# Optimization experiments

Measured on AMD Instinct MI355X. Metric: run time of the kernel, lower is better.

The kernel has to match this reference:

```python
import jax, jax.numpy as jnp
import numpy as np

TOKENS_PER_LAYER = 16  # v in rearrange 'b l (a v) -> b l a v'


def setup_inputs() -> dict:
    key = jax.random.key(0)
    k1, k2 = jax.random.split(key)
    vocab, embed_dim = 1024, 256
    x = jax.random.normal(k1, (64, 32, embed_dim * TOKENS_PER_LAYER), dtype=jnp.float32)
    # nn.Embedding init: uniform(-1/vocab, 1/vocab)
    emb_weight = jax.random.uniform(k2, (vocab, embed_dim), dtype=jnp.float32,
                                    minval=-1.0 / vocab, maxval=1.0 / vocab)
    return {"x": x, "emb_weight": emb_weight}


def reference(x, emb_weight):
    v = TOKENS_PER_LAYER
    b, l, av = x.shape
    a = av // v  # embed_dim
    # rearrange 'b l (a v) -> b l a v'
    z = x.reshape(b, l, a, v)
    # rearrange 'b l a v -> (b l v) a'
    z_flat = z.transpose(0, 1, 3, 2).reshape(b * l * v, a)
    # pairwise squared L2 distance via sum-of-squares + GEMM: [N, vocab]
    dist = (jnp.sum(z_flat * z_flat, axis=1, keepdims=True)
            + jnp.sum(emb_weight * emb_weight, axis=1)
            - 2.0 * (z_flat @ emb_weight.T))
    tokens = jnp.argmin(dist, axis=-1)  # [N] int
    # embedding gather, then rearrange '(b l v) e -> b l e v'
    z_q = emb_weight[tokens].reshape(b, l, v, a).transpose(0, 1, 3, 2)
    # straight-through decoder input: z + sg(z_q - z)
    decoder_input = z + jax.lax.stop_gradient(z_q - z)
    tokens = tokens.reshape(b, l, v)
    return z_q, decoder_input, tokens
```

## Files before the change

kernel.cpp:

```cpp
#include <hip/hip_runtime.h>


#define A_DIM 256
#define VOCAB 1024
#define NROWS 32768
#define ZQ_ELEMS ((size_t)8388608)
#define TAU_C 3.0e-4f
#define TAU_F 2.0e-4f

typedef _Float16 f16x8 __attribute__((ext_vector_type(8)));
typedef float f32x4 __attribute__((ext_vector_type(4)));

#define WS_EHT   ((size_t)0)
#define WS_ZH    ((size_t)524288)
#define WS_ESQ   ((size_t)17301504)
#define WS_ZSQ   ((size_t)17305600)
#define WS_NEED  ((size_t)17436672)


__global__ __launch_bounds__(256) void prep_fused(const float* __restrict__ x,
                                                  const float* __restrict__ emb,
                                                  _Float16* __restrict__ zh,
                                                  float* __restrict__ zsq,
                                                  float* __restrict__ esq,
                                                  _Float16* __restrict__ eht) {
    __shared__ float raw[A_DIM * 17];
    const int tid = threadIdx.x;
    if (blockIdx.x >= 2048) {
        const int blk = blockIdx.x - 2048;
        const int j = blk * 16 + (tid & 15);
        const int sub = tid >> 4;
        const float4* row = (const float4*)(emb + (size_t)j * A_DIM);
        #pragma unroll
        for (int t = 0; t < 2; ++t) {
            int kb = sub * 2 + t;
            float4 e0 = row[kb * 2], e1 = row[kb * 2 + 1];
            f16x8 hh;
            hh[0] = (_Float16)e0.x; hh[1] = (_Float16)e0.y; hh[2] = (_Float16)e0.z; hh[3] = (_Float16)e0.w;
            hh[4] = (_Float16)e1.x; hh[5] = (_Float16)e1.y; hh[6] = (_Float16)e1.z; hh[7] = (_Float16)e1.w;
            *(f16x8*)(eht + ((size_t)kb * 1024 + j) * 8) = hh;
        }
        if (sub == 0) {
            double s = 0.0;
            #pragma unroll 4
            for (int t = 0; t < A_DIM / 4; ++t) {
                float4 f = row[t];
                float sx = f.x * f.x, sy = f.y * f.y, sz = f.z * f.z, sw = f.w * f.w;
                s += (double)sx + (double)sy + (double)sz + (double)sw;
            }
            esq[j] = (float)s;
        }
        return;
    }
    const int bl = blockIdx.x;
    #pragma unroll
    for (int t = 0; t < 4; ++t) {
        int f4 = tid * 4 + t * 1024;
        float4 val = *(const float4*)(x + (size_t)bl * 4096 + f4);
        int a = f4 >> 4, v0 = f4 & 15;
        raw[a * 17 + v0 + 0] = val.x;
        raw[a * 17 + v0 + 1] = val.y;
        raw[a * 17 + v0 + 2] = val.z;
        raw[a * 17 + v0 + 3] = val.w;
    }
    __syncthreads();
    #pragma unroll
    for (int t = 0; t < 16; ++t) {
        int f = tid + t * 256;
        int v = f >> 8, a = f & 255;
        zh[((size_t)bl * 16 + v) * 256 + a] = (_Float16)raw[a * 17 + v];
    }
    if (tid < 16) {
        double s = 0.0;
        for (int a = 0; a < A_DIM; ++a) {
            float zf = raw[a * 17 + tid];
            float z2 = zf * zf;
            s += (double)z2;
        }
        zsq[bl * 16 + tid] = (float)s;
    }
}

__global__ __launch_bounds__(256) void mega_kernel(const _Float16* __restrict__ zh,
                                                   const _Float16* __restrict__ eht,
                                                   const float* __restrict__ esq_g,
                                                   const float* __restrict__ zsq,
                                                   const float* __restrict__ x,
                                                   const float* __restrict__ emb,
                                                   float* __restrict__ out) {
    __shared__ float t3buf[2][32][6];
    __shared__ float zrow[A_DIM];
    __shared__ float wv[4];
    __shared__ int   wi[4];
    __shared__ int rowtok[32], rowcls[32], rowc1[32], rowc2[32];

    const int tid = threadIdx.x;
    const int wq = tid >> 6;
    const int lane = tid & 63;
    const int q = lane >> 4;
    const int ln = lane & 15;
    const int g = wq & 1;
    const int h = wq >> 1;
    const int row0 = blockIdx.x * 32 + g * 16;
    const int cbase = h * 512;

    f16x8 afr[8];
    #pragma unroll
    for (int kt = 0; kt < 8; ++kt)
        afr[kt] = *(const f16x8*)(zh + (size_t)(row0 + ln) * 256 + kt * 32 + q * 8);

    const f16x8* ep[8];
    #pragma unroll
    for (int kt = 0; kt < 8; ++kt)
        ep[kt] = (const f16x8*)(eht + ((size_t)(kt * 4 + q) * 1024 + cbase + ln) * 8);

    float tv1[4], tv2[4], tv3[4];
    int   ti1[4], ti2[4], ti3[4];
    #pragma unroll
    for (int s = 0; s < 4; ++s) {
        tv1[s] = 3.0e38f; tv2[s] = 3.0e38f; tv3[s] = 3.0e38f;
        ti1[s] = 0; ti2[s] = 0; ti3[s] = 0;
    }

    for (int ch = 0; ch < 32; ++ch) {
        f16x8 bfr[8];
        #pragma unroll
        for (int kt = 0; kt < 8; ++kt)
            bfr[kt] = ep[kt][(size_t)ch * 16];
        f32x4 a0 = (f32x4){0.f, 0.f, 0.f, 0.f};
        f32x4 a1 = (f32x4){0.f, 0.f, 0.f, 0.f};
        #pragma unroll
        for (int kt = 0; kt < 4; ++kt)
            a0 = __builtin_amdgcn_mfma_f32_16x16x32_f16(afr[kt], bfr[kt], a0, 0, 0, 0);
        #pragma unroll
        for (int kt = 4; kt < 8; ++kt)
            a1 = __builtin_amdgcn_mfma_f32_16x16x32_f16(afr[kt], bfr[kt], a1, 0, 0, 0);
        const int cand = cbase + ch * 16 + ln;
        float es = esq_g[cand];
        #pragma unroll
        for (int reg = 0; reg < 4; ++reg) {
            float s = fmaf(-2.0f, a0[reg] + a1[reg], es);
            if (s < tv3[reg]) {
                if (s < tv2[reg]) {
                    tv3[reg] = tv2[reg]; ti3[reg] = ti2[reg];
                    if (s < tv1[reg]) {
                        tv2[reg] = tv1[reg]; ti2[reg] = ti1[reg];
                        tv1[reg] = s; ti1[reg] = cand;
                    } else { tv2[reg] = s; ti2[reg] = cand; }
                } else { tv3[reg] = s; ti3[reg] = cand; }
            }
        }
    }

    #pragma unroll
    for (int slot = 0; slot < 4; ++slot) {
        float v1 = tv1[slot], v2 = tv2[slot], v3 = tv3[slot];
        int i1 = ti1[slot], i2 = ti2[slot], i3 = ti3[slot];
        #pragma unroll
        for (int m = 1; m <= 8; m <<= 1) {
            float ov1 = __shfl_xor(v1, m); int oi1 = __shfl_xor(i1, m);
            float ov2 = __shfl_xor(v2, m); int oi2 = __shfl_xor(i2, m);
            float ov3 = __shfl_xor(v3, m); int oi3 = __shfl_xor(i3, m);
            #define INS3(ov, oi)                                                         \
                if (ov < v3 || (ov == v3 && oi < i3)) {                                  \
                    if (ov < v2 || (ov == v2 && oi < i2)) {                              \
                        v3 = v2; i3 = i2;                                                \
                        if (ov < v1 || (ov == v1 && oi < i1)) {                          \
                            v2 = v1; i2 = i1; v1 = ov; i1 = oi;                          \
                        } else { v2 = ov; i2 = oi; }                                     \
                    } else { v3 = ov; i3 = oi; }                                         \
                }
            INS3(ov1, oi1)
            INS3(ov2, oi2)
            INS3(ov3, oi3)
            #undef INS3
        }
        if (ln == 0) {
            int rl = g * 16 + q * 4 + slot;
            float* hp = &t3buf[h][rl][0];
            hp[0] = v1; hp[1] = __int_as_float(i1);
            hp[2] = v2; hp[3] = __int_as_float(i2);
            hp[4] = v3; hp[5] = __int_as_float(i3);
        }
    }
    __syncthreads();

    if (tid < 32) {
        const float* h0 = &t3buf[0][tid][0];
        const float* h1 = &t3buf[1][tid][0];
        float v1 = h0[0]; int i1 = __float_as_int(h0[1]);
        float v2 = h0[2]; int i2 = __float_as_int(h0[3]);
        float v3 = h0[4]; int i3 = __float_as_int(h0[5]);
        #pragma unroll
        for (int e = 0; e < 3; ++e) {
            float ov = h1[2 * e]; int oi = __float_as_int(h1[2 * e + 1]);
            if (ov < v3 || (ov == v3 && oi < i3)) {
                if (ov < v2 || (ov == v2 && oi < i2)) {
                    v3 = v2; i3 = i2;
                    if (ov < v1 || (ov == v1 && oi < i1)) {
                        v2 = v1; i2 = i1; v1 = ov; i1 = oi;
                    } else { v2 = ov; i2 = oi; }
                } else { v3 = ov; i3 = oi; }
            }
        }
        rowtok[tid] = i1;
        rowc1[tid] = i1;
        rowc2[tid] = i2;
        int cls = 0;
        if (v2 - v1 <= TAU_C) cls = (v3 - v1 > TAU_C) ? 1 : 2;
        rowcls[tid] = cls;
    }
    __syncthreads();

    for (int rl = 0; rl < 32; ++rl) {
        if (rowcls[rl] != 2) continue;
        const int r = blockIdx.x * 32 + rl;
        __syncthreads();
        zrow[tid] = x[(size_t)(r >> 4) * 4096 + (size_t)tid * 16 + (r & 15)];
        __syncthreads();
        const float4* e0 = (const float4*)(emb + (size_t)tid * 4 * A_DIM);
        double d0 = 0.0, d1 = 0.0, d2 = 0.0, d3 = 0.0;
        #pragma unroll 8
        for (int k4 = 0; k4 < A_DIM / 4; ++k4) {
            float4 zf = *(const float4*)&zrow[k4 * 4];
            double z0 = (double)zf.x, z1 = (double)zf.y;
            double z2 = (double)zf.z, z3 = (double)zf.w;
            float4 f0 = e0[k4];
            float4 f1 = e0[64 + k4];
            float4 f2 = e0[128 + k4];
            float4 f3 = e0[192 + k4];
            d0 = fma((double)f0.x, z0, d0); d0 = fma((double)f0.y, z1, d0);
            d0 = fma((double)f0.z, z2, d0); d0 = fma((double)f0.w, z3, d0);
            d1 = fma((double)f1.x, z0, d1); d1 = fma((double)f1.y, z1, d1);
            d1 = fma((double)f1.z, z2, d1); d1 = fma((double)f1.w, z3, d1);
            d2 = fma((double)f2.x, z0, d2); d2 = fma((double)f2.y, z1, d2);
            d2 = fma((double)f2.z, z2, d2); d2 = fma((double)f2.w, z3, d2);
            d3 = fma((double)f3.x, z0, d3); d3 = fma((double)f3.y, z1, d3);
            d3 = fma((double)f3.z, z2, d3); d3 = fma((double)f3.w, z3, d3);
        }
        const float zq = zsq[r];
        float bv = 3.0e38f; int bi = 0;
        double dd[4] = {d0, d1, d2, d3};
        #pragma unroll
        for (int cc = 0; cc < 4; ++cc) {
            int c = tid * 4 + cc;
            float A = zq + esq_g[c];
            float D = (float)(2.0 * dd[cc]);
            float s = A - D;
            if (s < bv) { bv = s; bi = c; }
        }
        #pragma unroll
        for (int m = 1; m < 64; m <<= 1) {
            float ov = __shfl_xor(bv, m); int oi = __shfl_xor(bi, m);
            if (ov < bv || (ov == bv && oi < bi)) { bv = ov; bi = oi; }
        }
        if (lane == 0) { wv[wq] = bv; wi[wq] = bi; }
        __syncthreads();
        if (tid == 0) {
            float BV = wv[0]; int BI = wi[0];
            #pragma unroll
            for (int t = 1; t < 4; ++t)
                if (wv[t] < BV || (wv[t] == BV && wi[t] < BI)) { BV = wv[t]; BI = wi[t]; }
            rowtok[rl] = BI;
        }
    }

    for (int rl = wq; rl < 32; rl += 4) {
        if (rowcls[rl] != 1) continue;
        const int r = blockIdx.x * 32 + rl;
        const int c1 = rowc1[rl], c2 = rowc2[rl];
        const float* xr = x + (size_t)(r >> 4) * 4096 + (r & 15);
        const float* e1 = emb + (size_t)c1 * A_DIM;
        const float* e2 = emb + (size_t)c2 * A_DIM;
        double d1 = 0.0, d2 = 0.0;
        #pragma unroll
        for (int k = 0; k < 4; ++k) {
            int a = lane + k * 64;
            double zv = (double)xr[a * 16];
            d1 = fma(zv, (double)e1[a], d1);
            d2 = fma(zv, (double)e2[a], d2);
        }
        #pragma unroll
        for (int m = 1; m < 64; m <<= 1) {
            d1 += __shfl_xor(d1, m);
            d2 += __shfl_xor(d2, m);
        }
        if (lane == 0) {
            float zq = zsq[r];
            float A1 = zq + esq_g[c1];
            float D1 = (float)(2.0 * d1);
            float s1 = A1 - D1;
            float A2 = zq + esq_g[c2];
            float D2 = (float)(2.0 * d2);
            float s2 = A2 - D2;
            int bi = (s2 < s1 || (s2 == s1 && c2 < c1)) ? c2 : c1;
            rowtok[rl] = bi;
        }
    }
    __syncthreads();

    const int a = tid;
    #pragma unroll
    for (int gg = 0; gg < 2; ++gg) {
        const int bl = blockIdx.x * 2 + gg;
        __align__(16) float hbuf[16];
        #pragma unroll
        for (int v = 0; v < 16; ++v)
            hbuf[v] = emb[(size_t)rowtok[gg * 16 + v] * A_DIM + a];
        size_t base = ((size_t)bl * A_DIM + a) * 16;
        float4* p0 = (float4*)(out + base);
        float4* p1 = (float4*)(out + ZQ_ELEMS + base);
        #pragma unroll
        for (int qq = 0; qq < 4; ++qq) {
            float4 val = *(float4*)&hbuf[qq * 4];
            p0[qq] = val;
            p1[qq] = val;
        }
    }
    if (tid < 32)
        out[2 * ZQ_ELEMS + (size_t)(blockIdx.x * 32 + tid)] = (float)rowtok[tid];
}


__global__ __launch_bounds__(256) void prep_f(const float* __restrict__ emb,
                                              float* __restrict__ e_sq32) {
    int j = blockIdx.x * 256 + threadIdx.x;
    if (j < VOCAB) {
        const float4* row = (const float4*)(emb + (size_t)j * A_DIM);
        double s = 0.0;
        #pragma unroll 4
        for (int t = 0; t < A_DIM / 4; ++t) {
            float4 f = row[t];
            float sx = f.x * f.x, sy = f.y * f.y, sz = f.z * f.z, sw = f.w * f.w;
            s += (double)sx + (double)sy + (double)sz + (double)sw;
        }
        e_sq32[j] = (float)s;
    }
}

#define FBM 64
#define FBN 256
#define FBK 32
struct SmemF {
    union {
        struct { float zs[FBK][FBM]; float es[FBK][FBN]; };
        float4 mbuf[FBM][32];
        struct { double zrow[A_DIM]; float rbest[256]; int ridx[256]; };
    };
    double zsqp_s[4][FBM];
    float  zsq[FBM];
    int    tok[FBM];
    int    flagrows[FBM];
    int    nflag;
};

__global__ __launch_bounds__(256, 2) void main_f(const float* __restrict__ x,
                                                 const float* __restrict__ emb,
                                                 const float* __restrict__ e_sq32,
                                                 float* __restrict__ out) {
    __shared__ SmemF sm;
    const int tid = threadIdx.x;
    const int tx = tid & 31;
    const int ty = tid >> 5;
    const int blk = blockIdx.x;
    const int row0 = blk * FBM;
    const int bl0 = row0 >> 4;
    const int zrow_id = tid & 63;
    const int zq4     = tid >> 6;

    if (tid == 0) sm.nflag = 0;
    float v1[8], v2[8];
    int   i1[8], i2[8];
    #pragma unroll
    for (int r = 0; r < 8; ++r) { v1[r] = 3.0e38f; v2[r] = 3.0e38f; i1[r] = 0; i2[r] = 0; }
    double zsqp = 0.0;
    float4 zpf[2];
    float4 epf[8];
    for (int ct = 0; ct < VOCAB / FBN; ++ct) {
        float acc[8][8];
        #pragma unroll
        for (int rr = 0; rr < 8; ++rr)
            #pragma unroll
            for (int cc = 0; cc < 8; ++cc) acc[rr][cc] = 0.0f;
        for (int kt = 0; kt < A_DIM / FBK; ++kt) {
            if (kt == 0) {
                #pragma unroll
                for (int t = 0; t < 2; ++t) {
                    int f = tid + t * 256;
                    int v4 = f & 3, g = (f >> 2) & 3, kk = f >> 4;
                    zpf[t] = *(const float4*)(x + (size_t)(bl0 + g) * 4096 + (kt * FBK + kk) * 16 + v4 * 4);
                }
                #pragma unroll
                for (int t = 0; t < 8; ++t) {
                    int f = tid + t * 256;
                    int c = f & 255, k4 = f >> 8;
                    epf[t] = *(const float4*)(emb + (size_t)(ct * FBN + c) * A_DIM + kt * FBK + k4 * 4);
                }
            }
            __syncthreads();
            #pragma unroll
            for (int t = 0; t < 2; ++t) {
                int f = tid + t * 256;
                int v4 = f & 3, g = (f >> 2) & 3, kk = f >> 4;
                *(float4*)&sm.zs[kk][g * 16 + v4 * 4] = zpf[t];
            }
            #pragma unroll
            for (int t = 0; t < 8; ++t) {
                int f = tid + t * 256;
                int c = f & 255, k4 = f >> 8;
                sm.es[k4 * 4 + 0][c] = epf[t].x;
                sm.es[k4 * 4 + 1][c] = epf[t].y;
                sm.es[k4 * 4 + 2][c] = epf[t].z;
                sm.es[k4 * 4 + 3][c] = epf[t].w;
            }
            __syncthreads();
            if (kt + 1 < A_DIM / FBK) {
                #pragma unroll
                for (int t = 0; t < 2; ++t) {
                    int f = tid + t * 256;
                    int v4 = f & 3, g = (f >> 2) & 3, kk = f >> 4;
                    zpf[t] = *(const float4*)(x + (size_t)(bl0 + g) * 4096 + ((kt + 1) * FBK + kk) * 16 + v4 * 4);
                }
                #pragma unroll
                for (int t = 0; t < 8; ++t) {
                    int f = tid + t * 256;
                    int c = f & 255, k4 = f >> 8;
                    epf[t] = *(const float4*)(emb + (size_t)(ct * FBN + c) * A_DIM + (kt + 1) * FBK + k4 * 4);
                }
            }
            if (ct == 0 && (kt >> 1) == zq4) {
                #pragma unroll
                for (int kk = 0; kk < FBK; ++kk) {
                    float zf = sm.zs[kk][zrow_id];
                    float zf2 = zf * zf;
                    zsqp += (double)zf2;
                }
            }
            #pragma unroll 2
            for (int kk = 0; kk < FBK; ++kk) {
                float4 za = *(float4*)&sm.zs[kk][ty * 4];
                float4 zb = *(float4*)&sm.zs[kk][32 + ty * 4];
                float4 ea = *(float4*)&sm.es[kk][tx * 4];
                float4 eb = *(float4*)&sm.es[kk][128 + tx * 4];
                float zv[8] = {za.x, za.y, za.z, za.w, zb.x, zb.y, zb.z, zb.w};
                float ev[8] = {ea.x, ea.y, ea.z, ea.w, eb.x, eb.y, eb.z, eb.w};
                #pragma unroll
                for (int rr = 0; rr < 8; ++rr)
                    #pragma unroll
                    for (int cc = 0; cc < 8; ++cc)
                        acc[rr][cc] = fmaf(zv[rr], ev[cc], acc[rr][cc]);
            }
        }
        if (ct == 0) {
            sm.zsqp_s[zq4][zrow_id] = zsqp;
            __syncthreads();
            if (tid < FBM)
                sm.zsq[tid] = (float)(sm.zsqp_s[0][tid] + sm.zsqp_s[1][tid]
                                    + sm.zsqp_s[2][tid] + sm.zsqp_s[3][tid]);
            __syncthreads();
        }
        float esqv[8];
        #pragma unroll
        for (int cc = 0; cc < 8; ++cc) {
            int c = ct * FBN + (cc >> 2) * 128 + tx * 4 + (cc & 3);
            esqv[cc] = e_sq32[c];
        }
        #pragma unroll
        for (int rr = 0; rr < 8; ++rr) {
            int R = (rr >> 2) * 32 + ty * 4 + (rr & 3);
            float zq = sm.zsq[R];
            #pragma unroll
            for (int cc = 0; cc < 8; ++cc) {
                int c = ct * FBN + (cc >> 2) * 128 + tx * 4 + (cc & 3);
                float A = zq + esqv[cc];
                float s = fmaf(-2.0f, acc[rr][cc], A);
                if (s < v1[rr]) { v2[rr] = v1[rr]; i2[rr] = i1[rr]; v1[rr] = s; i1[rr] = c; }
                else if (s < v2[rr]) { v2[rr] = s; i2[rr] = c; }
            }
        }
    }
    __syncthreads();
    #pragma unroll
    for (int rr = 0; rr < 8; ++rr) {
        int r = (rr >> 2) * 32 + ty * 4 + (rr & 3);
        float4 m;
        m.x = v1[rr]; m.y = __int_as_float(i1[rr]);
        m.z = v2[rr]; m.w = __int_as_float(i2[rr]);
        sm.mbuf[r][tx] = m;
    }
    __syncthreads();
    if (tid < FBM) {
        int r = tid;
        float V1 = 3.0e38f, V2 = 3.0e38f;
        int I1 = 0, I2 = 0;
        for (int t = 0; t < 32; ++t) {
            float4 m = sm.mbuf[r][t];
            float a1 = m.x; int a1i = __float_as_int(m.y);
            float a2 = m.z; int a2i = __float_as_int(m.w);
            if (a1 < V1 || (a1 == V1 && a1i < I1)) { V2 = V1; I2 = I1; V1 = a1; I1 = a1i; }
            else if (a1 < V2 || (a1 == V2 && a1i < I2)) { V2 = a1; I2 = a1i; }
            if (a2 < V1 || (a2 == V1 && a2i < I1)) { V2 = V1; I2 = I1; V1 = a2; I1 = a2i; }
            else if (a2 < V2 || (a2 == V2 && a2i < I2)) { V2 = a2; I2 = a2i; }
        }
        sm.tok[r] = I1;
        if (V2 - V1 <= TAU_F) {
            int pos = atomicAdd(&sm.nflag, 1);
            sm.flagrows[pos] = r;
        }
    }
    __syncthreads();
    const int nf = sm.nflag;
    for (int i = 0; i < nf; ++i) {
        const int rl = sm.flagrows[i];
        const int bl = bl0 + (rl >> 4);
        const int v  = rl & 15;
        const float zqrow = sm.zsq[rl];
        sm.zrow[tid] = (double)x[(size_t)bl * 4096 + (size_t)tid * 16 + v];
        __syncthreads();
        float bv = 3.0e38f; int bi = 0;
        #pragma unroll
        for (int cc = 0; cc < 4; ++cc) {
            int c = tid * 4 + cc;
            const float4* er = (const float4*)(emb + (size_t)c * A_DIM);
            double dot = 0.0;
            #pragma unroll 8
            for (int k4 = 0; k4 < A_DIM / 4; ++k4) {
                float4 f = er[k4];
                dot = fma((double)f.x, sm.zrow[k4 * 4 + 0], dot);
                dot = fma((double)f.y, sm.zrow[k4 * 4 + 1], dot);
                dot = fma((double)f.z, sm.zrow[k4 * 4 + 2], dot);
                dot = fma((double)f.w, sm.zrow[k4 * 4 + 3], dot);
            }
            float A = zqrow + e_sq32[c];
            float D = (float)(2.0 * dot);
            float s = A - D;
            if (s < bv) { bv = s; bi = c; }
        }
        sm.rbest[tid] = bv; sm.ridx[tid] = bi;
        __syncthreads();
        if (tid == 0) {
            float BV = sm.rbest[0]; int BI = sm.ridx[0];
            for (int t = 1; t < 256; ++t) {
                float vv = sm.rbest[t];
                if (vv < BV) { BV = vv; BI = sm.ridx[t]; }
            }
            sm.tok[rl] = BI;
        }
        __syncthreads();
    }
    if (tid < FBM) {
        out[2 * ZQ_ELEMS + (size_t)(row0 + tid)] = (float)sm.tok[tid];
    }
    __syncthreads();
    const int a = tid;
    for (int g = 0; g < 4; ++g) {
        __align__(16) float h[16];
        #pragma unroll
        for (int v = 0; v < 16; ++v) {
            h[v] = emb[(size_t)sm.tok[g * 16 + v] * A_DIM + a];
        }
        size_t base = ((size_t)(bl0 + g) * A_DIM + a) * 16;
        float4* p0 = (float4*)(out + base);
        float4* p1 = (float4*)(out + ZQ_ELEMS + base);
        #pragma unroll
        for (int qq = 0; qq < 4; ++qq) {
            float4 val = *(float4*)&h[qq * 4];
            p0[qq] = val;
            p1[qq] = val;
        }
    }
}

extern "C" void kernel_launch(void* const* d_in, const int* in_sizes, int n_in,
                              void* d_out, int out_size, void* d_ws, size_t ws_size,
                              hipStream_t stream) {
    (void)in_sizes; (void)n_in; (void)out_size;
    const float* x   = (const float*)d_in[0];
    const float* emb = (const float*)d_in[1];
    float* out = (float*)d_out;
    char* ws = (char*)d_ws;

    if (ws_size >= WS_NEED) {
        _Float16* eht = (_Float16*)(ws + WS_EHT);
        _Float16* zh  = (_Float16*)(ws + WS_ZH);
        float* esq    = (float*)(ws + WS_ESQ);
        float* zsq    = (float*)(ws + WS_ZSQ);

        prep_fused<<<2112, 256, 0, stream>>>(x, emb, zh, zsq, esq, eht);
        mega_kernel<<<1024, 256, 0, stream>>>(zh, eht, esq, zsq, x, emb, out);
    } else {
        float* e_sq32 = (float*)ws;
        prep_f<<<4, 256, 0, stream>>>(emb, e_sq32);
        main_f<<<512, 256, 0, stream>>>(x, emb, e_sq32, out);
    }
}
```

Before: 280.0 us.

## Split fused kernel into MFMA candidate search and separate finish kernel

The combined kernel is split in two. The first does the half-precision MFMA distance search and writes the top-2 candidates and an ambiguity class per row to a workspace buffer. A new finish kernel with 2048 blocks re-checks ambiguous rows in double precision and writes the gathered z_q and decoder outputs. Separating the work lets the MFMA kernel run with fewer LDS and register demands, so occupancy can rise, at the cost of an extra launch and a round trip of row info through global memory. The half-precision z writes in prep are also vectorized to 4-wide stores.

```diff
diff --git a/kernel.cpp b/kernel.cpp
--- a/kernel.cpp
+++ b/kernel.cpp
@@ -9,13 +9,15 @@
 #define TAU_F 2.0e-4f
 
 typedef _Float16 f16x8 __attribute__((ext_vector_type(8)));
+typedef _Float16 f16x4 __attribute__((ext_vector_type(4)));
 typedef float f32x4 __attribute__((ext_vector_type(4)));
 
 #define WS_EHT   ((size_t)0)
 #define WS_ZH    ((size_t)524288)
 #define WS_ESQ   ((size_t)17301504)
 #define WS_ZSQ   ((size_t)17305600)
-#define WS_NEED  ((size_t)17436672)
+#define WS_RINFO ((size_t)17436672)
+#define WS_NEED  ((size_t)17960960)
 
 
 __global__ __launch_bounds__(256) void prep_fused(const float* __restrict__ x,
@@ -65,10 +67,15 @@
     }
     __syncthreads();
     #pragma unroll
-    for (int t = 0; t < 16; ++t) {
-        int f = tid + t * 256;
-        int v = f >> 8, a = f & 255;
-        zh[((size_t)bl * 16 + v) * 256 + a] = (_Float16)raw[a * 17 + v];
+    for (int t = 0; t < 4; ++t) {
+        int p = tid + t * 256;
+        int v = p >> 6, a0 = (p & 63) * 4;
+        f16x4 hq;
+        hq[0] = (_Float16)raw[(a0 + 0) * 17 + v];
+        hq[1] = (_Float16)raw[(a0 + 1) * 17 + v];
+        hq[2] = (_Float16)raw[(a0 + 2) * 17 + v];
+        hq[3] = (_Float16)raw[(a0 + 3) * 17 + v];
+        *(f16x4*)(zh + ((size_t)bl * 16 + v) * 256 + a0) = hq;
     }
     if (tid < 16) {
         double s = 0.0;
@@ -81,19 +88,11 @@
     }
 }
 
-__global__ __launch_bounds__(256) void mega_kernel(const _Float16* __restrict__ zh,
+__global__ __launch_bounds__(256) void mfma_kernel(const _Float16* __restrict__ zh,
                                                    const _Float16* __restrict__ eht,
                                                    const float* __restrict__ esq_g,
-                                                   const float* __restrict__ zsq,
-                                                   const float* __restrict__ x,
-                                                   const float* __restrict__ emb,
-                                                   float* __restrict__ out) {
+                                                   int4* __restrict__ rowinfo) {
     __shared__ float t3buf[2][32][6];
-    __shared__ float zrow[A_DIM];
-    __shared__ float wv[4];
-    __shared__ int   wi[4];
-    __shared__ int rowtok[32], rowcls[32], rowc1[32], rowc2[32];
-
     const int tid = threadIdx.x;
     const int wq = tid >> 6;
     const int lane = tid & 63;
@@ -203,20 +202,39 @@
                 } else { v3 = ov; i3 = oi; }
             }
         }
-        rowtok[tid] = i1;
-        rowc1[tid] = i1;
-        rowc2[tid] = i2;
         int cls = 0;
         if (v2 - v1 <= TAU_C) cls = (v3 - v1 > TAU_C) ? 1 : 2;
-        rowcls[tid] = cls;
-    }
-    __syncthreads();
-
-    for (int rl = 0; rl < 32; ++rl) {
-        if (rowcls[rl] != 2) continue;
-        const int r = blockIdx.x * 32 + rl;
+        rowinfo[blockIdx.x * 32 + tid] = make_int4(i1, i2, cls, 0);
+    }
+}
+
+__global__ __launch_bounds__(256) void finish_kernel(const float* __restrict__ x,
+                                                     const float* __restrict__ emb,
+                                                     const float* __restrict__ esq,
+                                                     const float* __restrict__ zsq,
+                                                     const int4* __restrict__ rowinfo,
+                                                     float* __restrict__ out) {
+    __shared__ int4 ri[16];
+    __shared__ int ftok[16];
+    __shared__ float zrow[A_DIM];
+    __shared__ float wv[4];
+    __shared__ int   wi[4];
+    const int tid = threadIdx.x;
+    const int wq = tid >> 6, lane = tid & 63;
+    const int bl = blockIdx.x;
+
+    if (tid < 16) {
+        int4 e = rowinfo[bl * 16 + tid];
+        ri[tid] = e;
+        ftok[tid] = e.x;
+    }
+    __syncthreads();
+
+    for (int j = 0; j < 16; ++j) {
+        if (ri[j].z != 2) continue;
+        const int r = bl * 16 + j;
         __syncthreads();
-        zrow[tid] = x[(size_t)(r >> 4) * 4096 + (size_t)tid * 16 + (r & 15)];
+        zrow[tid] = x[(size_t)bl * 4096 + (size_t)tid * 16 + j];
         __syncthreads();
         const float4* e0 = (const float4*)(emb + (size_t)tid * 4 * A_DIM);
         double d0 = 0.0, d1 = 0.0, d2 = 0.0, d3 = 0.0;
@@ -244,7 +262,7 @@
         #pragma unroll
         for (int cc = 0; cc < 4; ++cc) {
             int c = tid * 4 + cc;
-            float A = zq + esq_g[c];
+            float A = zq + esq[c];
             float D = (float)(2.0 * dd[cc]);
             float s = A - D;
             if (s < bv) { bv = s; bi = c; }
@@ -261,15 +279,15 @@
             #pragma unroll
             for (int t = 1; t < 4; ++t)
                 if (wv[t] < BV || (wv[t] == BV && wi[t] < BI)) { BV = wv[t]; BI = wi[t]; }
-            rowtok[rl] = BI;
-        }
-    }
-
-    for (int rl = wq; rl < 32; rl += 4) {
-        if (rowcls[rl] != 1) continue;
-        const int r = blockIdx.x * 32 + rl;
-        const int c1 = rowc1[rl], c2 = rowc2[rl];
-        const float* xr = x + (size_t)(r >> 4) * 4096 + (r & 15);
+            ftok[j] = BI;
+        }
+    }
+
+    for (int j = wq; j < 16; j += 4) {
+        if (ri[j].z != 1) continue;
+        const int r = bl * 16 + j;
+        const int c1 = ri[j].x, c2 = ri[j].y;
+        const float* xr = x + (size_t)bl * 4096 + j;
         const float* e1 = emb + (size_t)c1 * A_DIM;
         const float* e2 = emb + (size_t)c2 * A_DIM;
         double d1 = 0.0, d2 = 0.0;
@@ -287,38 +305,34 @@
         }
         if (lane == 0) {
             float zq = zsq[r];
-            float A1 = zq + esq_g[c1];
+            float A1 = zq + esq[c1];
             float D1 = (float)(2.0 * d1);
             float s1 = A1 - D1;
-            float A2 = zq + esq_g[c2];
+            float A2 = zq + esq[c2];
             float D2 = (float)(2.0 * d2);
             float s2 = A2 - D2;
             int bi = (s2 < s1 || (s2 == s1 && c2 < c1)) ? c2 : c1;
-            rowtok[rl] = bi;
-        }
-    }
-    __syncthreads();
-
+            ftok[j] = bi;
+        }
+    }
+    __syncthreads();
+
+    if (tid < 16)
+        out[2 * ZQ_ELEMS + (size_t)(bl * 16 + tid)] = (float)ftok[tid];
     const int a = tid;
-    #pragma unroll
-    for (int gg = 0; gg < 2; ++gg) {
-        const int bl = blockIdx.x * 2 + gg;
-        __align__(16) float hbuf[16];
-        #pragma unroll
-        for (int v = 0; v < 16; ++v)
-            hbuf[v] = emb[(size_t)rowtok[gg * 16 + v] * A_DIM + a];
-        size_t base = ((size_t)bl * A_DIM + a) * 16;
-        float4* p0 = (float4*)(out + base);
-        float4* p1 = (float4*)(out + ZQ_ELEMS + base);
-        #pragma unroll
-        for (int qq = 0; qq < 4; ++qq) {
-            float4 val = *(float4*)&hbuf[qq * 4];
-            p0[qq] = val;
-            p1[qq] = val;
-        }
-    }
-    if (tid < 32)
-        out[2 * ZQ_ELEMS + (size_t)(blockIdx.x * 32 + tid)] = (float)rowtok[tid];
+    __align__(16) float hbuf[16];
+    #pragma unroll
+    for (int v = 0; v < 16; ++v)
+        hbuf[v] = emb[(size_t)ftok[v] * A_DIM + a];
+    size_t base = ((size_t)bl * A_DIM + a) * 16;
+    float4* p0 = (float4*)(out + base);
+    float4* p1 = (float4*)(out + ZQ_ELEMS + base);
+    #pragma unroll
+    for (int qq = 0; qq < 4; ++qq) {
+        float4 val = *(float4*)&hbuf[qq * 4];
+        p0[qq] = val;
+        p1[qq] = val;
+    }
 }
 
 
@@ -585,9 +599,11 @@
         _Float16* zh  = (_Float16*)(ws + WS_ZH);
         float* esq    = (float*)(ws + WS_ESQ);
         float* zsq    = (float*)(ws + WS_ZSQ);
+        int4* rinfo   = (int4*)(ws + WS_RINFO);
 
         prep_fused<<<2112, 256, 0, stream>>>(x, emb, zh, zsq, esq, eht);
-        mega_kernel<<<1024, 256, 0, stream>>>(zh, eht, esq, zsq, x, emb, out);
+        mfma_kernel<<<1024, 256, 0, stream>>>(zh, eht, esq, rinfo);
+        finish_kernel<<<2048, 256, 0, stream>>>(x, emb, esq, zsq, rinfo, out);
     } else {
         float* e_sq32 = (float*)ws;
         prep_f<<<4, 256, 0, stream>>>(emb, e_sq32);
```

Result: faster. 251.0 us (-10.3%).
